# Kernel tuning notes

Hardware: AMD Instinct MI355X
Metric: run time of the kernel (lower is better)

Reference implementation:

```python
import jax, jax.numpy as jnp
import numpy as np

N_UNITS = 512
H = 8
D_K = N_UNITS // H  # 64
B = 4
T = 1024


def setup_inputs() -> dict:
    key = jax.random.key(0)
    ks = jax.random.split(key, 10)
    s = 0.02
    return {
        "x": jax.random.normal(ks[0], (B * T, N_UNITS), dtype=jnp.float32),
        "pos_k": jax.random.normal(ks[1], (T, T, D_K), dtype=jnp.float32),
        "batch_size": B,
        "Wq": jax.random.normal(ks[2], (N_UNITS, N_UNITS), dtype=jnp.float32) * s,
        "bq": jax.random.normal(ks[3], (N_UNITS,), dtype=jnp.float32) * s,
        "Wk": jax.random.normal(ks[4], (N_UNITS, N_UNITS), dtype=jnp.float32) * s,
        "bk": jax.random.normal(ks[5], (N_UNITS,), dtype=jnp.float32) * s,
        "Wv": jax.random.normal(ks[6], (N_UNITS, N_UNITS), dtype=jnp.float32) * s,
        "bv": jax.random.normal(ks[7], (N_UNITS,), dtype=jnp.float32) * s,
        "Wo": jax.random.normal(ks[8], (N_UNITS, N_UNITS), dtype=jnp.float32) * s,
        "bo": jax.random.normal(ks[9], (N_UNITS,), dtype=jnp.float32) * s,
    }


def reference(x, pos_k, batch_size, Wq, bq, Wk, bk, Wv, bv, Wo, bo):
    # x: [B*T, n_units]; pos_k: [T, T, d_k]
    q = (x @ Wq + bq).reshape(batch_size, -1, H, D_K).transpose(0, 2, 1, 3)  # [B,h,T,d]
    k = (x @ Wk + bk).reshape(batch_size, -1, H, D_K).transpose(0, 2, 1, 3)
    v = (x @ Wv + bv).reshape(batch_size, -1, H, D_K).transpose(0, 2, 1, 3)
    att_score = jnp.einsum("bhqd,bhkd->bhqk", q, k)
    # relative-position score: per query position t, q[:,:,t] @ pos_k[t].T
    att_score_pos = jnp.einsum("bhqd,qkd->bhqk", q, pos_k)
    scores = (att_score + att_score_pos) / np.sqrt(D_K).astype(np.float32)
    att = jax.nn.softmax(scores, axis=3)  # dropout p=0 -> identity (eval)
    out = jnp.einsum("bhqk,bhkd->bhqd", att, v)  # [B,h,T,d]
    out = out.transpose(0, 2, 1, 3).reshape(-1, H * D_K)  # [B*T, n_units]
    return out @ Wo + bo
```

## Files before the change

kernel.cpp:

```cpp
#include <hip/hip_runtime.h>


#define TT 1024
#define DH 64
#define NH 8
#define NU 512

typedef __bf16 bf16;
typedef bf16 bf16x8 __attribute__((ext_vector_type(8)));
typedef bf16 bf16x4 __attribute__((ext_vector_type(4)));
typedef float f32x4 __attribute__((ext_vector_type(4)));

#define MFMA16(a, b, c) __builtin_amdgcn_mfma_f32_16x16x32_bf16(a, b, c, 0, 0, 0)

__global__ __launch_bounds__(256) void cvtx_k(const float* __restrict__ x,
                                              bf16* __restrict__ xb) {
  int i = blockIdx.x * 256 + threadIdx.x;
  float4 v = ((const float4*)x)[i];
  bf16x4 o = {(bf16)v.x, (bf16)v.y, (bf16)v.z, (bf16)v.w};
  ((bf16x4*)xb)[i] = o;
}

__global__ __launch_bounds__(256) void wtrans_k(const float* __restrict__ Wq,
                                                const float* __restrict__ Wk,
                                                const float* __restrict__ Wv,
                                                const float* __restrict__ Wo,
                                                bf16* __restrict__ wt) {
  int n = blockIdx.x * 256 + threadIdx.x;
  int k0 = blockIdx.y * 8;
  int w = blockIdx.z;
  const float* W = (w == 0) ? Wq : (w == 1) ? Wk : (w == 2) ? Wv : Wo;
  bf16x8 v;
#pragma unroll
  for (int j = 0; j < 8; j++) v[j] = (bf16)W[(size_t)(k0 + j) * NU + n];
  *(bf16x8*)(wt + ((size_t)w * NU + n) * NU + k0) = v;
}

__global__ __launch_bounds__(256) void qkv_k(
    const bf16* __restrict__ xb, const bf16* __restrict__ wt,
    const float* __restrict__ bq, const float* __restrict__ bk,
    const float* __restrict__ bv, bf16* __restrict__ Qb, bf16* __restrict__ Kb,
    bf16* __restrict__ Vt) {
  int tid = threadIdx.x, wid = tid >> 6, ln = tid & 63;
  int n15 = ln & 15, qd = ln >> 4;
  int n0 = blockIdx.x * 64, m0 = blockIdx.y * 64;
  int mrow = m0 + wid * 16 + n15;

  const f32x4 fz = {0.f, 0.f, 0.f, 0.f};
  f32x4 acc[3][4];
#pragma unroll
  for (int w = 0; w < 3; w++)
#pragma unroll
    for (int nt = 0; nt < 4; nt++) acc[w][nt] = fz;

  for (int k0 = 0; k0 < NU; k0 += 32) {
    bf16x8 a = *(const bf16x8*)(xb + (size_t)mrow * NU + k0 + qd * 8);
#pragma unroll
    for (int w = 0; w < 3; w++)
#pragma unroll
      for (int nt = 0; nt < 4; nt++) {
        bf16x8 b = *(const bf16x8*)(wt + ((size_t)w * NU + n0 + nt * 16 + n15) * NU +
                                    k0 + qd * 8);
        acc[w][nt] = MFMA16(a, b, acc[w][nt]);
      }
  }

  int bb = m0 >> 10;
  int tbase = (m0 & 1023) + wid * 16 + qd * 4;
  int hh = n0 >> 6;
#pragma unroll
  for (int nt = 0; nt < 4; nt++) {
    int d = nt * 16 + n15;
    float bqv = bq[n0 + d], bkv = bk[n0 + d], bvv = bv[n0 + d];
    bf16x4 vv;
#pragma unroll
    for (int r = 0; r < 4; r++) {
      int t = tbase + r;
      size_t qk_idx = ((size_t)(bb * NH + hh) * TT + t) * DH + d;
      Qb[qk_idx] = (bf16)(acc[0][nt][r] + bqv);
      Kb[qk_idx] = (bf16)(acc[1][nt][r] + bkv);
      vv[r] = (bf16)(acc[2][nt][r] + bvv);
    }
    *(bf16x4*)(Vt + ((size_t)(bb * NH + hh) * DH + d) * TT + tbase) = vv;
  }
}

__global__ __launch_bounds__(256) void pos_gemm_k(const float* __restrict__ pos,
                                                  const bf16* __restrict__ Qb,
                                                  bf16* __restrict__ biasS) {
  int tid = threadIdx.x, wid = tid >> 6, ln = tid & 63;
  int n15 = ln & 15, qd = ln >> 4;
  int t = blockIdx.y;
  int s0b = blockIdx.x * 128;

  __shared__ bf16 Qs[32 * 72];
  {
    int bh = tid >> 3, dc = (tid & 7) * 8;
    bf16x8 q = *(const bf16x8*)(Qb + ((size_t)bh * TT + t) * DH + dc);
    *(bf16x8*)(&Qs[bh * 72 + dc]) = q;
  }
  __syncthreads();

  bf16x8 aQ[2][2];
#pragma unroll
  for (int mt = 0; mt < 2; mt++)
#pragma unroll
    for (int kc = 0; kc < 2; kc++)
      aQ[mt][kc] = *(const bf16x8*)(&Qs[(mt * 16 + n15) * 72 + kc * 32 + qd * 8]);

  const f32x4 fz = {0.f, 0.f, 0.f, 0.f};
  f32x4 acc[2][2];
#pragma unroll
  for (int mt = 0; mt < 2; mt++)
#pragma unroll
    for (int ntl = 0; ntl < 2; ntl++) acc[mt][ntl] = fz;

#pragma unroll
  for (int ntl = 0; ntl < 2; ntl++) {
    int s = s0b + (wid * 2 + ntl) * 16 + n15;
    const float* pr = pos + ((size_t)t * TT + s) * DH + qd * 8;
#pragma unroll
    for (int kc = 0; kc < 2; kc++) {
      f32x4 u = __builtin_nontemporal_load((const f32x4*)(pr + kc * 32));
      f32x4 v = __builtin_nontemporal_load((const f32x4*)(pr + kc * 32 + 4));
      bf16x8 bB = {(bf16)u[0], (bf16)u[1], (bf16)u[2], (bf16)u[3],
                   (bf16)v[0], (bf16)v[1], (bf16)v[2], (bf16)v[3]};
#pragma unroll
      for (int mt = 0; mt < 2; mt++) acc[mt][ntl] = MFMA16(aQ[mt][kc], bB, acc[mt][ntl]);
    }
  }
#pragma unroll
  for (int mt = 0; mt < 2; mt++)
#pragma unroll
    for (int ntl = 0; ntl < 2; ntl++)
#pragma unroll
      for (int r = 0; r < 4; r++) {
        int s = s0b + (wid * 2 + ntl) * 16 + n15;
        int bh = mt * 16 + qd * 4 + r;
        biasS[((size_t)bh * TT + t) * TT + s] = (bf16)acc[mt][ntl][r];
      }
}

__global__ __launch_bounds__(256) void flash_k(const bf16* __restrict__ Qb,
                                               const bf16* __restrict__ Kb,
                                               const bf16* __restrict__ Vt,
                                               const bf16* __restrict__ biasS,
                                               bf16* __restrict__ att) {
  int tid = threadIdx.x, wid = tid >> 6, ln = tid & 63;
  int n15 = ln & 15, qd = ln >> 4;
  int bh = blockIdx.x;
  int t0 = blockIdx.y * 64 + wid * 16;
  const float SC = 0.18033688f;

  __shared__ bf16 Pl[4][16][40];

  bf16x8 bQ[2];
#pragma unroll
  for (int kc = 0; kc < 2; kc++)
    bQ[kc] = *(const bf16x8*)(Qb + ((size_t)bh * TT + t0 + n15) * DH + kc * 32 + qd * 8);

  const bf16* Kbase = Kb + (size_t)bh * TT * DH;
  const bf16* Vbase = Vt + (size_t)bh * DH * TT;
  const bf16* Bbase = biasS + ((size_t)bh * TT + t0 + n15) * TT;

  const f32x4 fz = {0.f, 0.f, 0.f, 0.f};
  f32x4 accO[4] = {fz, fz, fz, fz};
  f32x4 accL = fz;
  const bf16 one = (bf16)1.0f;
  const bf16x8 onesv = {one, one, one, one, one, one, one, one};

  bf16x8 Kf[2][4], Vf[2][4];
  bf16x4 Bf[4][2];

  auto ldKV = [&](int buf, int s0) {
#pragma unroll
    for (int mt = 0; mt < 2; mt++)
#pragma unroll
      for (int kc = 0; kc < 2; kc++)
        Kf[buf][mt * 2 + kc] =
            *(const bf16x8*)(Kbase + (size_t)(s0 + mt * 16 + n15) * DH + kc * 32 + qd * 8);
#pragma unroll
    for (int dt = 0; dt < 4; dt++)
      Vf[buf][dt] = *(const bf16x8*)(Vbase + (size_t)(dt * 16 + n15) * TT + s0 + qd * 8);
  };
  auto ldB = [&](int buf, int s0) {
#pragma unroll
    for (int mt = 0; mt < 2; mt++)
      Bf[buf][mt] = *(const bf16x4*)(Bbase + s0 + mt * 16 + qd * 4);
  };

  ldB(0, 0);
  ldB(1, 32);
  ldKV(0, 0);

#pragma unroll 4
  for (int it = 0; it < 32; it++) {
    int s0 = it * 32;
    ldKV((it + 1) & 1, (s0 + 32) & 1023);
    ldB((it + 2) & 3, (s0 + 64) & 1023);

    f32x4 accS[2] = {fz, fz};
#pragma unroll
    for (int mt = 0; mt < 2; mt++)
#pragma unroll
      for (int kc = 0; kc < 2; kc++)
        accS[mt] = MFMA16(Kf[it & 1][mt * 2 + kc], bQ[kc], accS[mt]);

#pragma unroll
    for (int mt = 0; mt < 2; mt++) {
      bf16x4 pb;
#pragma unroll
      for (int r = 0; r < 4; r++) {
        float p = __builtin_amdgcn_exp2f((accS[mt][r] + (float)Bf[it & 3][mt][r]) * SC);
        pb[r] = (bf16)p;
      }
      *(bf16x4*)(&Pl[wid][n15][mt * 16 + qd * 4]) = pb;
    }
    bf16x8 bP = *(const bf16x8*)(&Pl[wid][n15][qd * 8]);
    accL = MFMA16(onesv, bP, accL);
#pragma unroll
    for (int dt = 0; dt < 4; dt++) accO[dt] = MFMA16(Vf[it & 1][dt], bP, accO[dt]);
  }

  int bb = bh >> 3, hh = bh & 7;
  float rcp = 1.0f / accL[0];
#pragma unroll
  for (int dt = 0; dt < 4; dt++) {
    bf16x4 ov;
#pragma unroll
    for (int r = 0; r < 4; r++) ov[r] = (bf16)(accO[dt][r] * rcp);
    *(bf16x4*)(att + ((size_t)bb * TT + t0 + n15) * NU + hh * DH + dt * 16 + qd * 4) = ov;
  }
}

__global__ __launch_bounds__(256) void proj_k(const bf16* __restrict__ att,
                                              const bf16* __restrict__ wt,
                                              const float* __restrict__ bo,
                                              float* __restrict__ out) {
  int tid = threadIdx.x, wid = tid >> 6, ln = tid & 63;
  int n15 = ln & 15, qd = ln >> 4;
  int n0 = blockIdx.x * 64, m0 = blockIdx.y * 64;
  int mrow = m0 + wid * 16 + n15;

  const f32x4 fz = {0.f, 0.f, 0.f, 0.f};
  f32x4 acc[4] = {fz, fz, fz, fz};
  for (int k0 = 0; k0 < NU; k0 += 32) {
    bf16x8 a = *(const bf16x8*)(att + (size_t)mrow * NU + k0 + qd * 8);
#pragma unroll
    for (int nt = 0; nt < 4; nt++) {
      bf16x8 b = *(const bf16x8*)(wt + ((size_t)3 * NU + n0 + nt * 16 + n15) * NU +
                                  k0 + qd * 8);
      acc[nt] = MFMA16(a, b, acc[nt]);
    }
  }
#pragma unroll
  for (int nt = 0; nt < 4; nt++) {
    int col = n0 + nt * 16 + n15;
    float bov = bo[col];
#pragma unroll
    for (int r = 0; r < 4; r++) {
      int row = m0 + wid * 16 + qd * 4 + r;
      out[(size_t)row * NU + col] = acc[nt][r] + bov;
    }
  }
}

extern "C" void kernel_launch(void* const* d_in, const int* in_sizes, int n_in,
                              void* d_out, int out_size, void* d_ws, size_t ws_size,
                              hipStream_t stream) {
  const float* x = (const float*)d_in[0];
  const float* pos = (const float*)d_in[1];
  const float* Wq = (const float*)d_in[3];
  const float* bq = (const float*)d_in[4];
  const float* Wk = (const float*)d_in[5];
  const float* bk = (const float*)d_in[6];
  const float* Wv = (const float*)d_in[7];
  const float* bv = (const float*)d_in[8];
  const float* Wo = (const float*)d_in[9];
  const float* bo = (const float*)d_in[10];
  float* out = (float*)d_out;

  char* ws = (char*)d_ws;
  bf16* xb = (bf16*)(ws);
  bf16* wt = (bf16*)(ws + ((size_t)4 << 20));
  bf16* Qb = (bf16*)(ws + ((size_t)6 << 20));
  bf16* Kb = (bf16*)(ws + ((size_t)10 << 20));
  bf16* Vt = (bf16*)(ws + ((size_t)14 << 20));
  bf16* att = (bf16*)(ws + ((size_t)18 << 20));
  bf16* biasS = (bf16*)(ws + ((size_t)22 << 20));

  cvtx_k<<<2048, 256, 0, stream>>>(x, xb);
  wtrans_k<<<dim3(2, 64, 4), 256, 0, stream>>>(Wq, Wk, Wv, Wo, wt);
  qkv_k<<<dim3(8, 64), 256, 0, stream>>>(xb, wt, bq, bk, bv, Qb, Kb, Vt);
  pos_gemm_k<<<dim3(8, 1024), 256, 0, stream>>>(pos, Qb, biasS);
  flash_k<<<dim3(32, 16), 256, 0, stream>>>(Qb, Kb, Vt, biasS, att);
  proj_k<<<dim3(8, 64), 256, 0, stream>>>(att, wt, bo, out);
}
```

Before: 538.2 us.

## Store position-bias scores in MFMA-fragment-native tiled layout for flash kernel

The pos GEMM now swaps operand roles so each lane holds 8 consecutive bias values, and writes them as 16-byte vectors into a tiled layout that matches the flash kernel's per-lane fragment order. Before, it issued scattered 2-byte stores with a stride of a whole row. The flash kernel then reads one bf16x8 per iteration instead of two strided bf16x4 loads. This targets the write inefficiency of the 64MB bias intermediate and improves read coalescing. The indexing is more complex, and correctness depends on the new layout mapping matching the fragment order exactly.

```diff
diff --git a/kernel.cpp b/kernel.cpp
--- a/kernel.cpp
+++ b/kernel.cpp
@@ -87,7 +87,7 @@
 
 __global__ __launch_bounds__(256) void pos_gemm_k(const float* __restrict__ pos,
                                                   const bf16* __restrict__ Qb,
-                                                  bf16* __restrict__ biasS) {
+                                                  bf16* __restrict__ biasF) {
   int tid = threadIdx.x, wid = tid >> 6, ln = tid & 63;
   int n15 = ln & 15, qd = ln >> 4;
   int t = blockIdx.y;
@@ -96,55 +96,60 @@
   __shared__ bf16 Qs[32 * 72];
   {
     int bh = tid >> 3, dc = (tid & 7) * 8;
-    bf16x8 q = *(const bf16x8*)(Qb + ((size_t)bh * TT + t) * DH + dc);
-    *(bf16x8*)(&Qs[bh * 72 + dc]) = q;
+    *(bf16x8*)(&Qs[bh * 72 + dc]) =
+        *(const bf16x8*)(Qb + ((size_t)bh * TT + t) * DH + dc);
   }
   __syncthreads();
 
-  bf16x8 aQ[2][2];
-#pragma unroll
-  for (int mt = 0; mt < 2; mt++)
+  bf16x8 bQ[2][2];
+#pragma unroll
+  for (int bht = 0; bht < 2; bht++)
 #pragma unroll
     for (int kc = 0; kc < 2; kc++)
-      aQ[mt][kc] = *(const bf16x8*)(&Qs[(mt * 16 + n15) * 72 + kc * 32 + qd * 8]);
+      bQ[bht][kc] = *(const bf16x8*)(&Qs[(bht * 16 + n15) * 72 + kc * 32 + qd * 8]);
 
   const f32x4 fz = {0.f, 0.f, 0.f, 0.f};
   f32x4 acc[2][2];
 #pragma unroll
-  for (int mt = 0; mt < 2; mt++)
-#pragma unroll
-    for (int ntl = 0; ntl < 2; ntl++) acc[mt][ntl] = fz;
-
-#pragma unroll
-  for (int ntl = 0; ntl < 2; ntl++) {
-    int s = s0b + (wid * 2 + ntl) * 16 + n15;
-    const float* pr = pos + ((size_t)t * TT + s) * DH + qd * 8;
+  for (int stl = 0; stl < 2; stl++)
+#pragma unroll
+    for (int bht = 0; bht < 2; bht++) acc[stl][bht] = fz;
+
+  int sw = s0b + wid * 32;
+#pragma unroll
+  for (int stl = 0; stl < 2; stl++) {
+    const float* pr = pos + ((size_t)t * TT + sw + stl * 16 + n15) * DH + qd * 8;
 #pragma unroll
     for (int kc = 0; kc < 2; kc++) {
       f32x4 u = __builtin_nontemporal_load((const f32x4*)(pr + kc * 32));
       f32x4 v = __builtin_nontemporal_load((const f32x4*)(pr + kc * 32 + 4));
-      bf16x8 bB = {(bf16)u[0], (bf16)u[1], (bf16)u[2], (bf16)u[3],
+      bf16x8 aP = {(bf16)u[0], (bf16)u[1], (bf16)u[2], (bf16)u[3],
                    (bf16)v[0], (bf16)v[1], (bf16)v[2], (bf16)v[3]};
 #pragma unroll
-      for (int mt = 0; mt < 2; mt++) acc[mt][ntl] = MFMA16(aQ[mt][kc], bB, acc[mt][ntl]);
-    }
-  }
-#pragma unroll
-  for (int mt = 0; mt < 2; mt++)
-#pragma unroll
-    for (int ntl = 0; ntl < 2; ntl++)
-#pragma unroll
-      for (int r = 0; r < 4; r++) {
-        int s = s0b + (wid * 2 + ntl) * 16 + n15;
-        int bh = mt * 16 + qd * 4 + r;
-        biasS[((size_t)bh * TT + t) * TT + s] = (bf16)acc[mt][ntl][r];
-      }
+      for (int bht = 0; bht < 2; bht++)
+        acc[stl][bht] = MFMA16(aP, bQ[bht][kc], acc[stl][bht]);
+    }
+  }
+
+  int t16 = t >> 4, tin = t & 15, s32 = (s0b >> 5) + wid;
+#pragma unroll
+  for (int bht = 0; bht < 2; bht++) {
+    bf16x8 ov;
+#pragma unroll
+    for (int r = 0; r < 4; r++) {
+      ov[r] = (bf16)acc[0][bht][r];
+      ov[4 + r] = (bf16)acc[1][bht][r];
+    }
+    *(bf16x8*)(biasF +
+               (((size_t)(bht * 16 + n15) * 64 + t16) * 32 + s32) * 512 +
+               tin * 32 + qd * 8) = ov;
+  }
 }
 
 __global__ __launch_bounds__(256) void flash_k(const bf16* __restrict__ Qb,
                                                const bf16* __restrict__ Kb,
                                                const bf16* __restrict__ Vt,
-                                               const bf16* __restrict__ biasS,
+                                               const bf16* __restrict__ biasF,
                                                bf16* __restrict__ att) {
   int tid = threadIdx.x, wid = tid >> 6, ln = tid & 63;
   int n15 = ln & 15, qd = ln >> 4;
@@ -161,7 +166,8 @@
 
   const bf16* Kbase = Kb + (size_t)bh * TT * DH;
   const bf16* Vbase = Vt + (size_t)bh * DH * TT;
-  const bf16* Bbase = biasS + ((size_t)bh * TT + t0 + n15) * TT;
+  const bf16* Fbase = biasF + (((size_t)bh * 64 + (t0 >> 4)) * 32) * 512 +
+                      n15 * 32 + qd * 8;
 
   const f32x4 fz = {0.f, 0.f, 0.f, 0.f};
   f32x4 accO[4] = {fz, fz, fz, fz};
@@ -170,7 +176,7 @@
   const bf16x8 onesv = {one, one, one, one, one, one, one, one};
 
   bf16x8 Kf[2][4], Vf[2][4];
-  bf16x4 Bf[4][2];
+  bf16x8 Bf[4];
 
   auto ldKV = [&](int buf, int s0) {
 #pragma unroll
@@ -184,9 +190,7 @@
       Vf[buf][dt] = *(const bf16x8*)(Vbase + (size_t)(dt * 16 + n15) * TT + s0 + qd * 8);
   };
   auto ldB = [&](int buf, int s0) {
-#pragma unroll
-    for (int mt = 0; mt < 2; mt++)
-      Bf[buf][mt] = *(const bf16x4*)(Bbase + s0 + mt * 16 + qd * 4);
+    Bf[buf] = *(const bf16x8*)(Fbase + (size_t)(s0 >> 5) * 512);
   };
 
   ldB(0, 0);
@@ -211,7 +215,8 @@
       bf16x4 pb;
 #pragma unroll
       for (int r = 0; r < 4; r++) {
-        float p = __builtin_amdgcn_exp2f((accS[mt][r] + (float)Bf[it & 3][mt][r]) * SC);
+        float p = __builtin_amdgcn_exp2f(
+            (accS[mt][r] + (float)Bf[it & 3][mt * 4 + r]) * SC);
         pb[r] = (bf16)p;
       }
       *(bf16x4*)(&Pl[wid][n15][mt * 16 + qd * 4]) = pb;
@@ -287,12 +292,12 @@
   bf16* Kb = (bf16*)(ws + ((size_t)10 << 20));
   bf16* Vt = (bf16*)(ws + ((size_t)14 << 20));
   bf16* att = (bf16*)(ws + ((size_t)18 << 20));
-  bf16* biasS = (bf16*)(ws + ((size_t)22 << 20));
+  bf16* biasF = (bf16*)(ws + ((size_t)22 << 20));
 
   cvtx_k<<<2048, 256, 0, stream>>>(x, xb);
   wtrans_k<<<dim3(2, 64, 4), 256, 0, stream>>>(Wq, Wk, Wv, Wo, wt);
   qkv_k<<<dim3(8, 64), 256, 0, stream>>>(xb, wt, bq, bk, bv, Qb, Kb, Vt);
-  pos_gemm_k<<<dim3(8, 1024), 256, 0, stream>>>(pos, Qb, biasS);
-  flash_k<<<dim3(32, 16), 256, 0, stream>>>(Qb, Kb, Vt, biasS, att);
+  pos_gemm_k<<<dim3(8, 1024), 256, 0, stream>>>(pos, Qb, biasF);
+  flash_k<<<dim3(32, 16), 256, 0, stream>>>(Qb, Kb, Vt, biasF, att);
   proj_k<<<dim3(8, 64), 256, 0, stream>>>(att, wt, bo, out);
 }
```

After: 524.7 us. 2.5% less time.
